# Performance work log

Measured on AMD Instinct MI355X. Metric: run time of the kernel, lower is better.

## Reference

```python
import jax, jax.numpy as jnp
import numpy as np

B, T, C = 2, 4096, 768
H = 12
D = C // H  # head_dim = 64

def setup_inputs() -> dict:
    key = jax.random.key(0)
    ks = jax.random.split(key, 5)
    s = 1.0 / np.sqrt(C)
    return {
        "x": jax.random.normal(ks[0], (B, T, C), dtype=jnp.float32),
        "qkv_w": jax.random.normal(ks[1], (C, 3 * C), dtype=jnp.float32) * s,
        "qkv_b": jax.random.normal(ks[2], (3 * C,), dtype=jnp.float32) * 0.02,
        "out_w": jax.random.normal(ks[3], (C, C), dtype=jnp.float32) * s,
        "out_b": jax.random.normal(ks[4], (C,), dtype=jnp.float32) * 0.02,
    }

def reference(x, qkv_w, qkv_b, out_w, out_b):
    b, t, c = x.shape
    qkv = x @ qkv_w + qkv_b                      # [B,T,3C]
    q, k, v = jnp.split(qkv, 3, axis=-1)
    # [B,T,C] -> [B,H,T,D]
    q = q.reshape(b, t, H, D).transpose(0, 2, 1, 3)
    k = k.reshape(b, t, H, D).transpose(0, 2, 1, 3)
    v = v.reshape(b, t, H, D).transpose(0, 2, 1, 3)
    scale = 1.0 / np.sqrt(D)
    attn = jnp.einsum('bhqd,bhkd->bhqk', q, k) * scale  # [B,H,T,T]
    causal = jnp.tril(jnp.ones((t, t), dtype=bool))
    attn = jnp.where(causal, attn, -jnp.inf)
    attn = jax.nn.softmax(attn, axis=-1)
    y = jnp.einsum('bhqk,bhkd->bhqd', attn, v)           # [B,H,T,D]
    y = y.transpose(0, 2, 1, 3).reshape(b, t, c)
    return y @ out_w + out_b
```

## Files before the change

### kernel.cpp

```cpp
#include <hip/hip_runtime.h>
#include <hip/hip_bf16.h>

#define T_SEQ 4096
#define C_DIM 768
#define H_NUM 12
#define D_HEAD 64
#define N3    2304
#define BHN   24

typedef __bf16 bf16x8 __attribute__((ext_vector_type(8)));
typedef float  f32x4  __attribute__((ext_vector_type(4)));

__device__ inline unsigned short f2b(float f) {
    unsigned int x = __float_as_uint(f);
    unsigned int r = (x + 0x7FFFu + ((x >> 16) & 1u)) >> 16;
    return (unsigned short)r;
}

__device__ inline unsigned int pack_trunc(float lo, float hi) {
    return __builtin_amdgcn_perm(__float_as_uint(hi), __float_as_uint(lo), 0x07060302u);
}

__device__ inline void load_lds16(const unsigned short* g, unsigned short* l) {
    __builtin_amdgcn_global_load_lds(
        (const __attribute__((address_space(1))) unsigned int*)(g),
        (__attribute__((address_space(3))) unsigned int*)(l),
        16, 0, 0);
}

__device__ inline void transpose_tile(const float* __restrict__ in,
                                      unsigned short* __restrict__ out,
                                      unsigned short* Ts, int k0, int n0,
                                      int R, int Cc, int tid)
{
    #pragma unroll
    for (int it = 0; it < 4; ++it) {
        int idx = tid + it * 256;
        int r = idx >> 4, c4 = idx & 15;
        float4 v = *reinterpret_cast<const float4*>(&in[(size_t)(k0 + r) * Cc + n0 + c4 * 4]);
        Ts[(c4 * 4 + 0) * 72 + r] = f2b(v.x);
        Ts[(c4 * 4 + 1) * 72 + r] = f2b(v.y);
        Ts[(c4 * 4 + 2) * 72 + r] = f2b(v.z);
        Ts[(c4 * 4 + 3) * 72 + r] = f2b(v.w);
    }
    __syncthreads();
    #pragma unroll
    for (int it = 0; it < 2; ++it) {
        int idx = tid + it * 256;
        int row = idx >> 3, ch = idx & 7;
        *reinterpret_cast<uint4*>(&out[(size_t)(n0 + row) * R + k0 + ch * 8]) =
            *reinterpret_cast<const uint4*>(&Ts[row * 72 + ch * 8]);
    }
}

__global__ __launch_bounds__(256) void prep(
    const float* __restrict__ x, const float* __restrict__ qkv_w,
    const float* __restrict__ out_w,
    unsigned short* __restrict__ xb, unsigned short* __restrict__ wtq,
    unsigned short* __restrict__ wto)
{
    __shared__ unsigned short Ts[64 * 72];
    const int b = blockIdx.x, tid = threadIdx.x;
    if (b < 6144) {
        int idx = b * 256 + tid;
        float4 v = reinterpret_cast<const float4*>(x)[idx];
        ushort4 u;
        u.x = f2b(v.x); u.y = f2b(v.y); u.z = f2b(v.z); u.w = f2b(v.w);
        reinterpret_cast<ushort4*>(xb)[idx] = u;
    } else if (b < 6576) {
        int bb = b - 6144;
        transpose_tile(qkv_w, wtq, Ts, (bb % 12) * 64, (bb / 12) * 64, C_DIM, N3, tid);
    } else {
        int bb = b - 6576;
        transpose_tile(out_w, wto, Ts, (bb % 12) * 64, (bb / 12) * 64, C_DIM, C_DIM, tid);
    }
}

__global__ __launch_bounds__(256) void qkv_gemm(
    const unsigned short* __restrict__ xb, const unsigned short* __restrict__ wt,
    const float* __restrict__ bias,
    unsigned short* __restrict__ Q, unsigned short* __restrict__ K,
    unsigned short* __restrict__ Vt)
{
    __shared__ unsigned short SH[128 * 128];
    unsigned short* As = SH;
    unsigned short* Bs = SH + 128 * 64;
    const int tid  = threadIdx.x;
    const int m0   = blockIdx.x * 128;
    const int n0   = blockIdx.y * 128;
    const int lane = tid & 63;
    const int wv   = tid >> 6;
    const int wr   = wv >> 1, wc = wv & 1;
    const int quad = lane >> 4;
    const int lr   = lane & 15;
    const int srow = lane >> 3;
    const int dch  = (lane & 7) ^ srow;

    f32x4 acc[4][4] = {};

    for (int kk = 0; kk < C_DIM; kk += 64) {
        __syncthreads();
        #pragma unroll
        for (int i = 0; i < 4; ++i) {
            int inst = wv * 4 + i;
            int r = inst * 8 + srow;
            load_lds16(xb + (size_t)(m0 + r) * C_DIM + kk + dch * 8, As + inst * 512);
            load_lds16(wt + (size_t)(n0 + r) * C_DIM + kk + dch * 8, Bs + inst * 512);
        }
        __syncthreads();
        #pragma unroll
        for (int k2 = 0; k2 < 2; ++k2) {
            bf16x8 af[4], bf[4];
            #pragma unroll
            for (int mt = 0; mt < 4; ++mt)
                af[mt] = *reinterpret_cast<const bf16x8*>(
                    &As[(wr * 64 + mt * 16 + lr) * 64 + (((k2 * 4 + quad) ^ (lr & 7)) * 8)]);
            #pragma unroll
            for (int nt = 0; nt < 4; ++nt)
                bf[nt] = *reinterpret_cast<const bf16x8*>(
                    &Bs[(wc * 64 + nt * 16 + lr) * 64 + (((k2 * 4 + quad) ^ (lr & 7)) * 8)]);
            #pragma unroll
            for (int mt = 0; mt < 4; ++mt)
                #pragma unroll
                for (int nt = 0; nt < 4; ++nt)
                    acc[mt][nt] = __builtin_amdgcn_mfma_f32_16x16x32_bf16(af[mt], bf[nt], acc[mt][nt], 0, 0, 0);
        }
    }

    const int whichblk = n0 / C_DIM;
    if (whichblk == 2) {
        __syncthreads();
        #pragma unroll
        for (int nt = 0; nt < 4; ++nt) {
            int dp = wc * 64 + nt * 16 + lr;
            float bj = bias[n0 + dp];
            #pragma unroll
            for (int mt = 0; mt < 4; ++mt) {
                int t0 = wr * 64 + mt * 16 + quad * 4;
                ushort4 u;
                u.x = f2b(acc[mt][nt][0] + bj);
                u.y = f2b(acc[mt][nt][1] + bj);
                u.z = f2b(acc[mt][nt][2] + bj);
                u.w = f2b(acc[mt][nt][3] + bj);
                int cs = (t0 >> 2) ^ ((dp & 15) << 1);
                *reinterpret_cast<ushort4*>(&SH[dp * 128 + cs * 4]) = u;
            }
        }
        __syncthreads();
        const int bb = m0 >> 12;
        const int t_base = m0 & 4095;
        const int h_base = (n0 - 2 * C_DIM) >> 6;
        #pragma unroll
        for (int i = 0; i < 8; ++i) {
            int idx = i * 256 + tid;
            int row = idx >> 4, cc = idx & 15;
            int pc = ((2 * cc) ^ ((row & 15) << 1)) * 4;
            uint4 val = *reinterpret_cast<const uint4*>(&SH[row * 128 + pc]);
            int head = h_base + (row >> 6);
            int d = row & 63;
            *reinterpret_cast<uint4*>(
                &Vt[((size_t)(bb * H_NUM + head) * D_HEAD + d) * T_SEQ + t_base + cc * 8]) = val;
        }
    } else {
        const int head0 = ((n0 % C_DIM) + wc * 64) >> 6;
        #pragma unroll
        for (int nt = 0; nt < 4; ++nt) {
            int d = nt * 16 + lr;
            float bj = bias[n0 + wc * 64 + nt * 16 + lr];
            #pragma unroll
            for (int mt = 0; mt < 4; ++mt) {
                #pragma unroll
                for (int reg = 0; reg < 4; ++reg) {
                    int i = m0 + wr * 64 + mt * 16 + quad * 4 + reg;
                    int bb = i >> 12, t = i & 4095;
                    float val = acc[mt][nt][reg] + bj;
                    size_t base = (size_t)(bb * H_NUM + head0) * T_SEQ + t;
                    if (whichblk == 0)
                        Q[base * D_HEAD + d] = f2b(val * 0.18033688011f);
                    else
                        K[base * D_HEAD + d] = f2b(val);
                }
            }
        }
    }
}

__global__ __launch_bounds__(256, 3) void flash_attn(
    const unsigned short* __restrict__ Q, const unsigned short* __restrict__ K,
    const unsigned short* __restrict__ Vt, unsigned short* __restrict__ Y)
{
    __shared__ unsigned short Ks[64 * 64];
    __shared__ unsigned short Vs[64 * 64];
    __shared__ unsigned short Ps[64 * 72];
    const int tid  = threadIdx.x;
    const int lane = tid & 63;
    const int wv   = tid >> 6;
    const int quad = lane >> 4;
    const int lr   = lane & 15;
    const int srow = lane >> 3;
    const int dch  = (lane & 7) ^ srow;

    const int bid = blockIdx.x;
    const int qt  = 31 - (bid / BHN);
    const int bh  = bid % BHN;
    const int q0  = qt * 128;
    const int diag0 = 2 * qt;

    const unsigned short* Qb = Q  + (size_t)bh * T_SEQ * D_HEAD;
    const unsigned short* Kb = K  + (size_t)bh * T_SEQ * D_HEAD;
    const unsigned short* Vb = Vt + (size_t)bh * D_HEAD * T_SEQ;

    bf16x8 bQ[2][2];
    #pragma unroll
    for (int h = 0; h < 2; ++h)
        #pragma unroll
        for (int k2 = 0; k2 < 2; ++k2)
            bQ[h][k2] = *reinterpret_cast<const bf16x8*>(
                &Qb[(size_t)(q0 + h * 64 + wv * 16 + lr) * D_HEAD + k2 * 32 + quad * 8]);

    f32x4 oacc[2][4] = {};
    float l_[2] = {0.f, 0.f};

    unsigned short* Pw = &Ps[(wv * 16) * 72];

    for (int kt = 0; kt <= diag0 + 1; ++kt) {
        __syncthreads();
        #pragma unroll
        for (int i = 0; i < 2; ++i) {
            int inst = wv * 2 + i;
            int r = inst * 8 + srow;
            load_lds16(Kb + (size_t)(kt * 64 + r) * D_HEAD + dch * 8, Ks + inst * 512);
            load_lds16(Vb + (size_t)r * T_SEQ + kt * 64 + dch * 8, Vs + inst * 512);
        }
        __syncthreads();

        bf16x8 aK[4][2], aV[4][2];
        #pragma unroll
        for (int mt = 0; mt < 4; ++mt)
            #pragma unroll
            for (int k2 = 0; k2 < 2; ++k2) {
                aK[mt][k2] = *reinterpret_cast<const bf16x8*>(
                    &Ks[(mt * 16 + lr) * 64 + (((k2 * 4 + quad) ^ (lr & 7)) * 8)]);
                aV[mt][k2] = *reinterpret_cast<const bf16x8*>(
                    &Vs[(mt * 16 + lr) * 64 + (((k2 * 4 + quad) ^ (lr & 7)) * 8)]);
            }

        #pragma unroll
        for (int h = 0; h < 2; ++h) {
            if (h == 0 && kt > diag0) continue;
            f32x4 st[4];
            #pragma unroll
            for (int mt = 0; mt < 4; ++mt) {
                f32x4 a = {};
                a = __builtin_amdgcn_mfma_f32_16x16x32_bf16(aK[mt][0], bQ[h][0], a, 0, 0, 0);
                a = __builtin_amdgcn_mfma_f32_16x16x32_bf16(aK[mt][1], bQ[h][1], a, 0, 0, 0);
                st[mt] = a;
            }
            const int qg = q0 + h * 64 + wv * 16 + lr;
            if (kt == diag0 + h) {
                #pragma unroll
                for (int mt = 0; mt < 4; ++mt)
                    #pragma unroll
                    for (int reg = 0; reg < 4; ++reg)
                        if (kt * 64 + mt * 16 + quad * 4 + reg > qg) st[mt][reg] = -INFINITY;
            }
            #pragma unroll
            for (int mt = 0; mt < 4; ++mt)
                #pragma unroll
                for (int reg = 0; reg < 4; ++reg) {
                    float p = exp2f(st[mt][reg]);
                    st[mt][reg] = p;
                    l_[h] += p;
                }
            #pragma unroll
            for (int mt = 0; mt < 4; ++mt) {
                uint2 u;
                u.x = pack_trunc(st[mt][0], st[mt][1]);
                u.y = pack_trunc(st[mt][2], st[mt][3]);
                *reinterpret_cast<uint2*>(&Pw[lr * 72 + mt * 16 + quad * 4]) = u;
            }
            bf16x8 bP0 = *reinterpret_cast<const bf16x8*>(&Pw[lr * 72 + quad * 8]);
            bf16x8 bP1 = *reinterpret_cast<const bf16x8*>(&Pw[lr * 72 + 32 + quad * 8]);
            #pragma unroll
            for (int dt = 0; dt < 4; ++dt) {
                oacc[h][dt] = __builtin_amdgcn_mfma_f32_16x16x32_bf16(aV[dt][0], bP0, oacc[h][dt], 0, 0, 0);
                oacc[h][dt] = __builtin_amdgcn_mfma_f32_16x16x32_bf16(aV[dt][1], bP1, oacc[h][dt], 0, 0, 0);
            }
        }
    }

    const int bb = bh / H_NUM, hh = bh % H_NUM;
    #pragma unroll
    for (int h = 0; h < 2; ++h) {
        float lt = l_[h];
        lt += __shfl_xor(lt, 16);
        lt += __shfl_xor(lt, 32);
        float inv = 1.f / lt;
        int q = q0 + h * 64 + wv * 16 + lr;
        #pragma unroll
        for (int dt = 0; dt < 4; ++dt) {
            ushort4 u;
            u.x = f2b(oacc[h][dt][0] * inv);
            u.y = f2b(oacc[h][dt][1] * inv);
            u.z = f2b(oacc[h][dt][2] * inv);
            u.w = f2b(oacc[h][dt][3] * inv);
            *reinterpret_cast<ushort4*>(
                &Y[(size_t)(bb * T_SEQ + q) * C_DIM + hh * 64 + dt * 16 + quad * 4]) = u;
        }
    }
}

__global__ __launch_bounds__(256) void out_gemm(
    const unsigned short* __restrict__ Y, const unsigned short* __restrict__ wt,
    const float* __restrict__ bias, float* __restrict__ out)
{
    __shared__ unsigned short As[128 * 64];
    __shared__ unsigned short Bs[64 * 64];
    const int tid  = threadIdx.x;
    const int m0   = blockIdx.x * 128;
    const int n0   = blockIdx.y * 64;
    const int lane = tid & 63;
    const int wv   = tid >> 6;
    const int wr   = wv >> 1, wc = wv & 1;
    const int quad = lane >> 4;
    const int lr   = lane & 15;
    const int srow = lane >> 3;
    const int dch  = (lane & 7) ^ srow;

    f32x4 acc[4][2] = {};

    for (int kk = 0; kk < C_DIM; kk += 64) {
        __syncthreads();
        #pragma unroll
        for (int i = 0; i < 4; ++i) {
            int inst = wv * 4 + i;
            int r = inst * 8 + srow;
            load_lds16(Y + (size_t)(m0 + r) * C_DIM + kk + dch * 8, As + inst * 512);
        }
        #pragma unroll
        for (int i = 0; i < 2; ++i) {
            int inst = wv * 2 + i;
            int r = inst * 8 + srow;
            load_lds16(wt + (size_t)(n0 + r) * C_DIM + kk + dch * 8, Bs + inst * 512);
        }
        __syncthreads();
        #pragma unroll
        for (int k2 = 0; k2 < 2; ++k2) {
            bf16x8 af[4], bf[2];
            #pragma unroll
            for (int mt = 0; mt < 4; ++mt)
                af[mt] = *reinterpret_cast<const bf16x8*>(
                    &As[(wr * 64 + mt * 16 + lr) * 64 + (((k2 * 4 + quad) ^ (lr & 7)) * 8)]);
            #pragma unroll
            for (int nt = 0; nt < 2; ++nt)
                bf[nt] = *reinterpret_cast<const bf16x8*>(
                    &Bs[(wc * 32 + nt * 16 + lr) * 64 + (((k2 * 4 + quad) ^ (lr & 7)) * 8)]);
            #pragma unroll
            for (int mt = 0; mt < 4; ++mt)
                #pragma unroll
                for (int nt = 0; nt < 2; ++nt)
                    acc[mt][nt] = __builtin_amdgcn_mfma_f32_16x16x32_bf16(af[mt], bf[nt], acc[mt][nt], 0, 0, 0);
        }
    }

    #pragma unroll
    for (int nt = 0; nt < 2; ++nt) {
        int j = n0 + wc * 32 + nt * 16 + lr;
        float bj = bias[j];
        #pragma unroll
        for (int mt = 0; mt < 4; ++mt)
            #pragma unroll
            for (int reg = 0; reg < 4; ++reg) {
                int i = m0 + wr * 64 + mt * 16 + quad * 4 + reg;
                out[(size_t)i * C_DIM + j] = acc[mt][nt][reg] + bj;
            }
    }
}

extern "C" void kernel_launch(void* const* d_in, const int* in_sizes, int n_in,
                              void* d_out, int out_size, void* d_ws, size_t ws_size,
                              hipStream_t stream) {
    const float* x     = (const float*)d_in[0];
    const float* qkv_w = (const float*)d_in[1];
    const float* qkv_b = (const float*)d_in[2];
    const float* out_w = (const float*)d_in[3];
    const float* out_b = (const float*)d_in[4];
    float* out = (float*)d_out;

    unsigned short* xb  = (unsigned short*)d_ws;
    unsigned short* wtq = xb  + (size_t)8192 * 768;
    unsigned short* wto = wtq + (size_t)2304 * 768;
    unsigned short* Qs  = wto + (size_t)768 * 768;
    unsigned short* Kg  = Qs  + (size_t)BHN * T_SEQ * D_HEAD;
    unsigned short* Vt  = Kg  + (size_t)BHN * T_SEQ * D_HEAD;
    unsigned short* Y   = xb;

    prep      <<<6720, 256, 0, stream>>>(x, qkv_w, out_w, xb, wtq, wto);
    qkv_gemm  <<<dim3(64, 18), 256, 0, stream>>>(xb, wtq, qkv_b, Qs, Kg, Vt);
    flash_attn<<<dim3(32 * BHN), 256, 0, stream>>>(Qs, Kg, Vt, Y);
    out_gemm  <<<dim3(64, 12), 256, 0, stream>>>(Y, wto, out_b, out);
}
```

Measured before the change: 248.7 us.

## Double-buffer K/V tiles in flash attention and compute row sums via MFMA

Double-buffers the K and V LDS tiles so the next key block's global-to-LDS load is issued before the current block is computed, which drops one barrier per iteration. Splits the P staging buffer per half so both query halves' QK, exp2 and PV stages can interleave. The softmax denominator is now accumulated with an MFMA against a ones vector on the bf16-rounded P, replacing the scalar adds and cross-lane shuffles. LDS use roughly doubles, which may reduce the number of resident blocks per CU.

New measurement: 230.1 us. -7.5%, faster.

```diff
diff --git a/kernel.cpp b/kernel.cpp
--- a/kernel.cpp
+++ b/kernel.cpp
@@ -189,9 +189,9 @@
     const unsigned short* __restrict__ Q, const unsigned short* __restrict__ K,
     const unsigned short* __restrict__ Vt, unsigned short* __restrict__ Y)
 {
-    __shared__ unsigned short Ks[64 * 64];
-    __shared__ unsigned short Vs[64 * 64];
-    __shared__ unsigned short Ps[64 * 72];
+    __shared__ unsigned short Ks[2][64 * 64];
+    __shared__ unsigned short Vs[2][64 * 64];
+    __shared__ unsigned short Ps[2][64 * 72];
     const int tid  = threadIdx.x;
     const int lane = tid & 63;
     const int wv   = tid >> 6;
@@ -205,6 +205,7 @@
     const int bh  = bid % BHN;
     const int q0  = qt * 128;
     const int diag0 = 2 * qt;
+    const int last  = diag0 + 1;
 
     const unsigned short* Qb = Q  + (size_t)bh * T_SEQ * D_HEAD;
     const unsigned short* Kb = K  + (size_t)bh * T_SEQ * D_HEAD;
@@ -218,84 +219,141 @@
             bQ[h][k2] = *reinterpret_cast<const bf16x8*>(
                 &Qb[(size_t)(q0 + h * 64 + wv * 16 + lr) * D_HEAD + k2 * 32 + quad * 8]);
 
+    bf16x8 ones;
+    #pragma unroll
+    for (int i = 0; i < 8; ++i) ones[i] = (__bf16)1.0f;
+    const f32x4 zf = {};
+
     f32x4 oacc[2][4] = {};
-    float l_[2] = {0.f, 0.f};
-
-    unsigned short* Pw = &Ps[(wv * 16) * 72];
-
-    for (int kt = 0; kt <= diag0 + 1; ++kt) {
-        __syncthreads();
-        #pragma unroll
-        for (int i = 0; i < 2; ++i) {
-            int inst = wv * 2 + i;
-            int r = inst * 8 + srow;
-            load_lds16(Kb + (size_t)(kt * 64 + r) * D_HEAD + dch * 8, Ks + inst * 512);
-            load_lds16(Vb + (size_t)r * T_SEQ + kt * 64 + dch * 8, Vs + inst * 512);
-        }
-        __syncthreads();
-
-        bf16x8 aK[4][2], aV[4][2];
+    f32x4 lacc[2] = {};
+
+    unsigned short* Pw0 = &Ps[0][(wv * 16) * 72];
+    unsigned short* Pw1 = &Ps[1][(wv * 16) * 72];
+
+    #pragma unroll
+    for (int i = 0; i < 2; ++i) {
+        int inst = wv * 2 + i;
+        int r = inst * 8 + srow;
+        load_lds16(Kb + (size_t)r * D_HEAD + dch * 8, Ks[0] + inst * 512);
+        load_lds16(Vb + (size_t)r * T_SEQ + dch * 8, Vs[0] + inst * 512);
+    }
+
+    for (int kt = 0; kt <= last; ++kt) {
+        const int buf = kt & 1;
+        __syncthreads();
+
+        if (kt < last) {
+            #pragma unroll
+            for (int i = 0; i < 2; ++i) {
+                int inst = wv * 2 + i;
+                int r = inst * 8 + srow;
+                load_lds16(Kb + (size_t)((kt + 1) * 64 + r) * D_HEAD + dch * 8,
+                           Ks[buf ^ 1] + inst * 512);
+                load_lds16(Vb + (size_t)r * T_SEQ + (kt + 1) * 64 + dch * 8,
+                           Vs[buf ^ 1] + inst * 512);
+            }
+        }
+
+        const bool doh0 = (kt <= diag0);
+
+        bf16x8 aK[4][2];
         #pragma unroll
         for (int mt = 0; mt < 4; ++mt)
             #pragma unroll
-            for (int k2 = 0; k2 < 2; ++k2) {
+            for (int k2 = 0; k2 < 2; ++k2)
                 aK[mt][k2] = *reinterpret_cast<const bf16x8*>(
-                    &Ks[(mt * 16 + lr) * 64 + (((k2 * 4 + quad) ^ (lr & 7)) * 8)]);
+                    &Ks[buf][(mt * 16 + lr) * 64 + (((k2 * 4 + quad) ^ (lr & 7)) * 8)]);
+
+        f32x4 st0[4], st1[4];
+        #pragma unroll
+        for (int mt = 0; mt < 4; ++mt) {
+            st1[mt] = __builtin_amdgcn_mfma_f32_16x16x32_bf16(aK[mt][0], bQ[1][0], zf, 0, 0, 0);
+            st1[mt] = __builtin_amdgcn_mfma_f32_16x16x32_bf16(aK[mt][1], bQ[1][1], st1[mt], 0, 0, 0);
+        }
+        if (doh0) {
+            #pragma unroll
+            for (int mt = 0; mt < 4; ++mt) {
+                st0[mt] = __builtin_amdgcn_mfma_f32_16x16x32_bf16(aK[mt][0], bQ[0][0], zf, 0, 0, 0);
+                st0[mt] = __builtin_amdgcn_mfma_f32_16x16x32_bf16(aK[mt][1], bQ[0][1], st0[mt], 0, 0, 0);
+            }
+        }
+
+        if (kt == diag0) {
+            int qg = q0 + wv * 16 + lr;
+            #pragma unroll
+            for (int mt = 0; mt < 4; ++mt)
+                #pragma unroll
+                for (int reg = 0; reg < 4; ++reg)
+                    if (kt * 64 + mt * 16 + quad * 4 + reg > qg) st0[mt][reg] = -INFINITY;
+        }
+        if (kt == last) {
+            int qg = q0 + 64 + wv * 16 + lr;
+            #pragma unroll
+            for (int mt = 0; mt < 4; ++mt)
+                #pragma unroll
+                for (int reg = 0; reg < 4; ++reg)
+                    if (kt * 64 + mt * 16 + quad * 4 + reg > qg) st1[mt][reg] = -INFINITY;
+        }
+
+        #pragma unroll
+        for (int mt = 0; mt < 4; ++mt) {
+            #pragma unroll
+            for (int reg = 0; reg < 4; ++reg)
+                st1[mt][reg] = __builtin_amdgcn_exp2f(st1[mt][reg]);
+            uint2 u;
+            u.x = pack_trunc(st1[mt][0], st1[mt][1]);
+            u.y = pack_trunc(st1[mt][2], st1[mt][3]);
+            *reinterpret_cast<uint2*>(&Pw1[lr * 72 + mt * 16 + quad * 4]) = u;
+        }
+        if (doh0) {
+            #pragma unroll
+            for (int mt = 0; mt < 4; ++mt) {
+                #pragma unroll
+                for (int reg = 0; reg < 4; ++reg)
+                    st0[mt][reg] = __builtin_amdgcn_exp2f(st0[mt][reg]);
+                uint2 u;
+                u.x = pack_trunc(st0[mt][0], st0[mt][1]);
+                u.y = pack_trunc(st0[mt][2], st0[mt][3]);
+                *reinterpret_cast<uint2*>(&Pw0[lr * 72 + mt * 16 + quad * 4]) = u;
+            }
+        }
+
+        bf16x8 aV[4][2];
+        #pragma unroll
+        for (int mt = 0; mt < 4; ++mt)
+            #pragma unroll
+            for (int k2 = 0; k2 < 2; ++k2)
                 aV[mt][k2] = *reinterpret_cast<const bf16x8*>(
-                    &Vs[(mt * 16 + lr) * 64 + (((k2 * 4 + quad) ^ (lr & 7)) * 8)]);
-            }
-
-        #pragma unroll
-        for (int h = 0; h < 2; ++h) {
-            if (h == 0 && kt > diag0) continue;
-            f32x4 st[4];
-            #pragma unroll
-            for (int mt = 0; mt < 4; ++mt) {
-                f32x4 a = {};
-                a = __builtin_amdgcn_mfma_f32_16x16x32_bf16(aK[mt][0], bQ[h][0], a, 0, 0, 0);
-                a = __builtin_amdgcn_mfma_f32_16x16x32_bf16(aK[mt][1], bQ[h][1], a, 0, 0, 0);
-                st[mt] = a;
-            }
-            const int qg = q0 + h * 64 + wv * 16 + lr;
-            if (kt == diag0 + h) {
-                #pragma unroll
-                for (int mt = 0; mt < 4; ++mt)
-                    #pragma unroll
-                    for (int reg = 0; reg < 4; ++reg)
-                        if (kt * 64 + mt * 16 + quad * 4 + reg > qg) st[mt][reg] = -INFINITY;
-            }
-            #pragma unroll
-            for (int mt = 0; mt < 4; ++mt)
-                #pragma unroll
-                for (int reg = 0; reg < 4; ++reg) {
-                    float p = exp2f(st[mt][reg]);
-                    st[mt][reg] = p;
-                    l_[h] += p;
-                }
-            #pragma unroll
-            for (int mt = 0; mt < 4; ++mt) {
-                uint2 u;
-                u.x = pack_trunc(st[mt][0], st[mt][1]);
-                u.y = pack_trunc(st[mt][2], st[mt][3]);
-                *reinterpret_cast<uint2*>(&Pw[lr * 72 + mt * 16 + quad * 4]) = u;
-            }
-            bf16x8 bP0 = *reinterpret_cast<const bf16x8*>(&Pw[lr * 72 + quad * 8]);
-            bf16x8 bP1 = *reinterpret_cast<const bf16x8*>(&Pw[lr * 72 + 32 + quad * 8]);
+                    &Vs[buf][(mt * 16 + lr) * 64 + (((k2 * 4 + quad) ^ (lr & 7)) * 8)]);
+
+        if (doh0) {
+            bf16x8 bP0 = *reinterpret_cast<const bf16x8*>(&Pw0[lr * 72 + quad * 8]);
+            bf16x8 bP1 = *reinterpret_cast<const bf16x8*>(&Pw0[lr * 72 + 32 + quad * 8]);
             #pragma unroll
             for (int dt = 0; dt < 4; ++dt) {
-                oacc[h][dt] = __builtin_amdgcn_mfma_f32_16x16x32_bf16(aV[dt][0], bP0, oacc[h][dt], 0, 0, 0);
-                oacc[h][dt] = __builtin_amdgcn_mfma_f32_16x16x32_bf16(aV[dt][1], bP1, oacc[h][dt], 0, 0, 0);
-            }
+                oacc[0][dt] = __builtin_amdgcn_mfma_f32_16x16x32_bf16(aV[dt][0], bP0, oacc[0][dt], 0, 0, 0);
+                oacc[0][dt] = __builtin_amdgcn_mfma_f32_16x16x32_bf16(aV[dt][1], bP1, oacc[0][dt], 0, 0, 0);
+            }
+            lacc[0] = __builtin_amdgcn_mfma_f32_16x16x32_bf16(ones, bP0, lacc[0], 0, 0, 0);
+            lacc[0] = __builtin_amdgcn_mfma_f32_16x16x32_bf16(ones, bP1, lacc[0], 0, 0, 0);
+        }
+        {
+            bf16x8 bP0 = *reinterpret_cast<const bf16x8*>(&Pw1[lr * 72 + quad * 8]);
+            bf16x8 bP1 = *reinterpret_cast<const bf16x8*>(&Pw1[lr * 72 + 32 + quad * 8]);
+            #pragma unroll
+            for (int dt = 0; dt < 4; ++dt) {
+                oacc[1][dt] = __builtin_amdgcn_mfma_f32_16x16x32_bf16(aV[dt][0], bP0, oacc[1][dt], 0, 0, 0);
+                oacc[1][dt] = __builtin_amdgcn_mfma_f32_16x16x32_bf16(aV[dt][1], bP1, oacc[1][dt], 0, 0, 0);
+            }
+            lacc[1] = __builtin_amdgcn_mfma_f32_16x16x32_bf16(ones, bP0, lacc[1], 0, 0, 0);
+            lacc[1] = __builtin_amdgcn_mfma_f32_16x16x32_bf16(ones, bP1, lacc[1], 0, 0, 0);
         }
     }
 
     const int bb = bh / H_NUM, hh = bh % H_NUM;
     #pragma unroll
     for (int h = 0; h < 2; ++h) {
-        float lt = l_[h];
-        lt += __shfl_xor(lt, 16);
-        lt += __shfl_xor(lt, 32);
-        float inv = 1.f / lt;
+        float inv = 1.f / lacc[h][0];
         int q = q0 + h * 64 + wv * 16 + lr;
         #pragma unroll
         for (int dt = 0; dt < 4; ++dt) {
```
